# Optimization experiments

Hardware: AMD Instinct MI355X
Metric: run time of the kernel (lower is better)

## Reference

```python
import jax, jax.numpy as jnp
import numpy as np

HIGHEST = jax.lax.Precision.HIGHEST
KEY_CHUNK_SIZE = 4096 * 4  # hard-coded in the module's __call__
HEADS = 8
DIM_HEAD = 64


def _query_chunk_size(num_q: int) -> int:
    # replicates the module's static chunk-size selection
    if num_q % 64 == 0:
        return num_q // 64
    if num_q % 16 == 0:
        return num_q // 16
    if num_q % 4 == 0:
        return num_q // 4
    return num_q


def _me_attention(q, k, v, q_chunk: int, k_chunk: int):
    # q, k, v: (S, H, D) where H here is the flattened batch*heads axis
    S, H, D = q.shape
    num_kv = k.shape[0]
    k_chunk = min(k_chunk, num_kv)
    q = q / jnp.sqrt(jnp.asarray(D, q.dtype))
    kc = k.reshape(-1, k_chunk, H, D)          # (nk, kc, H, D)
    vc = v.reshape(-1, k_chunk, H, v.shape[-1])

    def per_qchunk(qch):  # qch: (qc, H, D)
        def summarize(args):
            kch, vch = args
            s = jnp.einsum('qhd,khd->qhk', qch, kch, precision=HIGHEST)
            m = jax.lax.stop_gradient(jnp.max(s, axis=-1, keepdims=True))
            e = jnp.exp(s - m)
            ev = jnp.einsum('khf,qhk->qhf', vch, e, precision=HIGHEST)
            return ev, e.sum(axis=-1), m[..., 0]
        evs, ews, ms = jax.lax.map(summarize, (kc, vc))  # stacked over key chunks
        gm = jnp.max(ms, axis=0)                # (qc, H) global running max
        sc = jnp.exp(ms - gm)                   # (nk, qc, H) rescale factors
        num = (evs * sc[..., None]).sum(axis=0)
        den = (ews * sc).sum(axis=0)
        return num / den[..., None]

    qs = q.reshape(-1, q_chunk, H, D)
    out = jax.lax.map(per_qchunk, qs)           # (nq, qc, H, F)
    return out.reshape(S, H, -1)


def _forward(hidden_states, w_q, w_k, w_v, w_out, b_out):
    B, S, Dm = hidden_states.shape
    H, dh = HEADS, DIM_HEAD
    q = hidden_states @ w_q
    k = hidden_states @ w_k
    v = hidden_states @ w_v

    def to_heads(t):  # (B,S,H*dh) -> (B*H, S, dh)
        return t.reshape(B, S, H, dh).transpose(0, 2, 1, 3).reshape(B * H, S, dh)

    qs, ks, vs = to_heads(q), to_heads(k), to_heads(v)
    # module transposes to (S, B*H, dh) before memory-efficient attention
    qcs = _query_chunk_size(S)
    attn = _me_attention(qs.transpose(1, 0, 2), ks.transpose(1, 0, 2),
                         vs.transpose(1, 0, 2), qcs, KEY_CHUNK_SIZE)
    attn = attn.transpose(1, 0, 2)  # (B*H, S, dh)
    attn = attn.reshape(B, H, S, dh).transpose(0, 2, 1, 3).reshape(B, S, H * dh)
    return attn @ w_out + b_out


def setup_inputs() -> dict:
    key = jax.random.key(0)
    ks = jax.random.split(key, 6)
    B, S, Dm = 2, 8192, 512
    inner = HEADS * DIM_HEAD  # 512
    return {
        'hidden_states': jax.random.normal(ks[0], (B, S, Dm), dtype=jnp.float32),
        'w_q': jax.random.normal(ks[1], (Dm, inner), dtype=jnp.float32) * 0.02,
        'w_k': jax.random.normal(ks[2], (Dm, inner), dtype=jnp.float32) * 0.02,
        'w_v': jax.random.normal(ks[3], (Dm, inner), dtype=jnp.float32) * 0.02,
        'w_out': jax.random.normal(ks[4], (inner, Dm), dtype=jnp.float32) * 0.02,
        'b_out': jnp.zeros((Dm,), dtype=jnp.float32),
    }


def reference(hidden_states, w_q, w_k, w_v, w_out, b_out):
    return _forward(hidden_states, w_q, w_k, w_v, w_out, b_out)
```

## Files before the change

### kernel.cpp

```cpp
#include <hip/hip_runtime.h>
#include <stdint.h>

typedef unsigned short u16;
typedef __attribute__((ext_vector_type(8))) short short8;
typedef __attribute__((ext_vector_type(4))) short short4v;
typedef __attribute__((ext_vector_type(4))) float f32x4;

#define MFMA16(a, b, c) __builtin_amdgcn_mfma_f32_16x16x16bf16_1k(a, b, c, 0, 0, 0)
#define MFMA32(a, b, c) __builtin_amdgcn_mfma_f32_16x16x32_bf16(a, b, c, 0, 0, 0)

#if __has_builtin(__builtin_amdgcn_exp2f)
#define EXP2F(x) __builtin_amdgcn_exp2f(x)
#else
#define EXP2F(x) exp2f(x)
#endif

#define ASYNC16(G, L)                                                            \
    __builtin_amdgcn_global_load_lds((const __attribute__((address_space(1))) void*)(const void*)(G), \
                                     (__attribute__((address_space(3))) void*)(void*)(L), 16, 0, 0)

__device__ __forceinline__ u16 f2bf(float f) {
    union { float f; uint32_t u; } c; c.f = f;
    uint32_t r = (c.u + 0x7fffu + ((c.u >> 16) & 1u)) >> 16;
    return (u16)r;
}

__global__ __launch_bounds__(256) void k_convert_x(const float* __restrict__ X, u16* __restrict__ Xb) {
    int idx = blockIdx.x * 256 + threadIdx.x;
    float4 v = ((const float4*)X)[idx];
    union { u16 s[4]; uint2 v; } u;
    u.s[0] = f2bf(v.x); u.s[1] = f2bf(v.y); u.s[2] = f2bf(v.z); u.s[3] = f2bf(v.w);
    ((uint2*)Xb)[idx] = u.v;
}

__global__ __launch_bounds__(256) void k_convert_w(const float* __restrict__ W0, const float* __restrict__ W1,
                                                   const float* __restrict__ W2, const float* __restrict__ W3,
                                                   u16* __restrict__ Wt) {
    __shared__ u16 T[64][72];
    const float* W = (blockIdx.z == 0) ? W0 : (blockIdx.z == 1) ? W1 : (blockIdx.z == 2) ? W2 : W3;
    int k0 = blockIdx.x * 64, n0 = blockIdx.y * 64;
    int t = threadIdx.x;
    for (int i = 0; i < 4; i++) {
        int id = t + i * 256;
        int row = id >> 4, c4 = (id & 15) * 4;
        float4 v = *(const float4*)(W + (size_t)(k0 + row) * 512 + n0 + c4);
        union { u16 s[4]; uint2 v; } u;
        u.s[0] = f2bf(v.x); u.s[1] = f2bf(v.y); u.s[2] = f2bf(v.z); u.s[3] = f2bf(v.w);
        *(uint2*)&T[row][c4] = u.v;
    }
    __syncthreads();
    u16* O = Wt + (size_t)blockIdx.z * 512 * 512;
    for (int i = 0; i < 2; i++) {
        int id = t + i * 256;
        int row = id >> 3, c8 = (id & 7) * 8;
        union { u16 s[8]; uint4 v; } tmp;
        for (int j = 0; j < 8; j++) tmp.s[j] = T[c8 + j][row];
        *(uint4*)(O + (size_t)(n0 + row) * 512 + k0 + c8) = tmp.v;
    }
}

__global__ __launch_bounds__(256) void k_gemm_qkv(const u16* __restrict__ X, const u16* __restrict__ Wt,
                                                  u16* __restrict__ Q, u16* __restrict__ K, u16* __restrict__ V) {
    __shared__ u16 As[128][40];
    __shared__ u16 Bs[128][40];
    const int t = threadIdx.x;
    const int wave = t >> 6, lane = t & 63, quad = lane >> 4, l16 = lane & 15;
    const int wm = (wave >> 1) * 64, wn = (wave & 1) * 64;
    const int m0 = blockIdx.x * 128, n0 = blockIdx.y * 128;
    const u16* Bt = Wt + (size_t)blockIdx.z * 262144;
    const f32x4 fz = {0.f, 0.f, 0.f, 0.f};
    f32x4 acc[4][4];
    for (int i = 0; i < 4; i++) for (int j = 0; j < 4; j++) acc[i][j] = fz;
    for (int k0 = 0; k0 < 512; k0 += 32) {
        __syncthreads();
        for (int i = 0; i < 2; i++) {
            int id = t + i * 256;
            int row = id >> 2, c8 = (id & 3) * 8;
            *(uint4*)&As[row][c8] = *(const uint4*)(X + (size_t)(m0 + row) * 512 + k0 + c8);
            *(uint4*)&Bs[row][c8] = *(const uint4*)(Bt + (size_t)(n0 + row) * 512 + k0 + c8);
        }
        __syncthreads();
        short8 af[4], bf[4];
        for (int mt = 0; mt < 4; mt++) af[mt] = *(const short8*)&As[wm + mt * 16 + l16][quad * 8];
        for (int nt = 0; nt < 4; nt++) bf[nt] = *(const short8*)&Bs[wn + nt * 16 + l16][quad * 8];
        for (int mt = 0; mt < 4; mt++)
            for (int nt = 0; nt < 4; nt++)
                acc[mt][nt] = MFMA32(af[mt], bf[nt], acc[mt][nt]);
    }
    const float scale = (blockIdx.z == 0) ? 0.18033688011112042f : 1.0f;
    u16* Out = (blockIdx.z == 0) ? Q : (blockIdx.z == 1) ? K : V;
    for (int mt = 0; mt < 4; mt++)
        for (int nt = 0; nt < 4; nt++)
            for (int r = 0; r < 4; r++) {
                int m = m0 + wm + mt * 16 + quad * 4 + r;
                int n = n0 + wn + nt * 16 + l16;
                int b = m >> 13, s = m & 8191, h = n >> 6, d = n & 63;
                Out[((size_t)((b * 8 + h) * 8192 + s)) * 64 + d] = f2bf(acc[mt][nt][r] * scale);
            }
}

__global__ __launch_bounds__(256) void k_transpose_v(const u16* __restrict__ V, u16* __restrict__ Vt) {
    __shared__ u16 T[64][72];
    int s0 = blockIdx.x * 64, bh = blockIdx.y;
    int t = threadIdx.x;
    for (int i = 0; i < 2; i++) {
        int id = t + i * 256, row = id >> 3, c8 = (id & 7) * 8;
        *(uint4*)&T[row][c8] = *(const uint4*)(V + ((size_t)bh * 8192 + s0 + row) * 64 + c8);
    }
    __syncthreads();
    for (int i = 0; i < 2; i++) {
        int id = t + i * 256, row = id >> 3, c8 = (id & 7) * 8;
        union { u16 s[8]; uint4 v; } tmp;
        for (int j = 0; j < 8; j++) tmp.s[j] = T[c8 + j][row];
        *(uint4*)(Vt + ((size_t)bh * 64 + row) * 8192 + s0 + c8) = tmp.v;
    }
}

__global__ __launch_bounds__(512, 4) void k_flash(const u16* __restrict__ Q, const u16* __restrict__ K,
                                                  const u16* __restrict__ Vt, u16* __restrict__ Attn) {
    __shared__ u16 KsAll[2][4096];
    __shared__ u16 VsAll[2][4096];
    const int t = threadIdx.x;
    const int wave = t >> 6, lane = t & 63, quad = lane >> 4, l16 = lane & 15;
    const int l7 = l16 & 7;
    const int qblk = blockIdx.x, bh = blockIdx.y;
    const int b = bh >> 3, h = bh & 7;
    const int q0g = qblk * 256;
    const int mq = wave * 32;
    const u16* Qb = Q + ((size_t)bh * 8192 + q0g) * 64;
    const u16* Kb = K + (size_t)bh * 8192 * 64;
    const u16* Vb = Vt + (size_t)bh * 64 * 8192;

    const int rA = ((l16 & 12) << 1) + (l16 & 3);

    const int r0 = t >> 3;
    const int x0K = ((t & 7) ^ ((r0 & 3) | ((r0 & 8) >> 1))) * 8;
    const int x0V = ((t & 7) ^ (r0 & 7)) * 8;
    const u16* gK0 = Kb + r0 * 64 + x0K;
    const u16* gV0 = Vb + (size_t)r0 * 8192 + x0V;
    u16* lK = &KsAll[0][0] + t * 8;
    u16* lV = &VsAll[0][0] + t * 8;

    auto prefetch = [&](int it, int buf) {
        ASYNC16(gK0 + it * 4096, lK + buf * 4096);
        ASYNC16(gV0 + it * 64,   lV + buf * 4096);
    };

    short8 qf[2][2];
    for (int mt = 0; mt < 2; mt++)
        for (int ks = 0; ks < 2; ks++)
            qf[mt][ks] = *(const short8*)(Qb + (size_t)(mq + mt * 16 + l16) * 64 + ks * 32 + quad * 8);

    const f32x4 fz = {0.f, 0.f, 0.f, 0.f};
    f32x4 o[2][4];
    float l_i[2] = {0.f, 0.f};
    for (int mt = 0; mt < 2; mt++) for (int nt = 0; nt < 4; nt++) o[mt][nt] = fz;

    prefetch(0, 0);

    auto body = [&](int it, int buf) {
        __syncthreads();
        if (it != 127) prefetch(it + 1, buf ^ 1);
        const u16* KsB = &KsAll[buf][0];
        const u16* VsB = &VsAll[buf][0];

        f32x4 scA[2][2], scB[2][2];
        for (int kg = 0; kg < 2; kg++) {
            const u16* KgA = KsB + kg * 2048 + rA * 64;
            const u16* KgB = KgA + 4 * 64;
            short8 a0 = *(const short8*)(KgA + ((0 * 4 + quad) ^ l7) * 8);
            short8 a1 = *(const short8*)(KgA + ((1 * 4 + quad) ^ l7) * 8);
            short8 b0 = *(const short8*)(KgB + ((0 * 4 + quad) ^ l7) * 8);
            short8 b1 = *(const short8*)(KgB + ((1 * 4 + quad) ^ l7) * 8);
            scA[0][kg] = MFMA32(a0, qf[0][0], fz);
            scA[1][kg] = MFMA32(a0, qf[1][0], fz);
            scB[0][kg] = MFMA32(b0, qf[0][0], fz);
            scB[1][kg] = MFMA32(b0, qf[1][0], fz);
            scA[0][kg] = MFMA32(a1, qf[0][1], scA[0][kg]);
            scA[1][kg] = MFMA32(a1, qf[1][1], scA[1][kg]);
            scB[0][kg] = MFMA32(b1, qf[0][1], scB[0][kg]);
            scB[1][kg] = MFMA32(b1, qf[1][1], scB[1][kg]);
        }

        short8 pf[2][2];
        for (int mt = 0; mt < 2; mt++)
            for (int kg = 0; kg < 2; kg++) {
                union { float f; uint32_t u; } eA0, eA1, eA2, eA3, eB0, eB1, eB2, eB3;
                eA0.f = EXP2F(scA[mt][kg][0]);
                eA1.f = EXP2F(scA[mt][kg][1]);
                eA2.f = EXP2F(scA[mt][kg][2]);
                eA3.f = EXP2F(scA[mt][kg][3]);
                eB0.f = EXP2F(scB[mt][kg][0]);
                eB1.f = EXP2F(scB[mt][kg][1]);
                eB2.f = EXP2F(scB[mt][kg][2]);
                eB3.f = EXP2F(scB[mt][kg][3]);
                l_i[mt] += ((eA0.f + eA1.f) + (eA2.f + eA3.f)) + ((eB0.f + eB1.f) + (eB2.f + eB3.f));
                union { uint32_t u[4]; short8 s; } pk;
                pk.u[0] = __builtin_amdgcn_perm(eA1.u, eA0.u, 0x07060302);
                pk.u[1] = __builtin_amdgcn_perm(eA3.u, eA2.u, 0x07060302);
                pk.u[2] = __builtin_amdgcn_perm(eB1.u, eB0.u, 0x07060302);
                pk.u[3] = __builtin_amdgcn_perm(eB3.u, eB2.u, 0x07060302);
                pf[mt][kg] = pk.s;
            }

        for (int kg = 0; kg < 2; kg++)
            for (int nt = 0; nt < 4; nt++) {
                short8 vf = *(const short8*)(VsB + nt * 1024 + l16 * 64 + (((kg * 4 + quad) ^ l7) * 8));
                o[0][nt] = MFMA32(pf[0][kg], vf, o[0][nt]);
                o[1][nt] = MFMA32(pf[1][kg], vf, o[1][nt]);
            }
    };

    for (int it2 = 0; it2 < 64; it2++) {
        body(2 * it2, 0);
        body(2 * it2 + 1, 1);
    }

    for (int mt = 0; mt < 2; mt++) {
        float l = l_i[mt];
        l += __shfl_xor(l, 16);
        l += __shfl_xor(l, 32);
        float inv = 1.0f / l;
        float invC[4];
        for (int r = 0; r < 4; r++) invC[r] = __shfl(inv, quad * 4 + r);
        for (int nt = 0; nt < 4; nt++)
            for (int r = 0; r < 4; r++) {
                int sg = q0g + mq + mt * 16 + quad * 4 + r;
                int n = h * 64 + nt * 16 + l16;
                Attn[((size_t)(b * 8192 + sg)) * 512 + n] = f2bf(o[mt][nt][r] * invC[r]);
            }
    }
}

__global__ __launch_bounds__(256) void k_gemm_out(const u16* __restrict__ A, const u16* __restrict__ Wot,
                                                  const float* __restrict__ bias, float* __restrict__ Out) {
    __shared__ u16 As[128][40];
    __shared__ u16 Bs[128][40];
    const int t = threadIdx.x;
    const int wave = t >> 6, lane = t & 63, quad = lane >> 4, l16 = lane & 15;
    const int wm = (wave >> 1) * 64, wn = (wave & 1) * 64;
    const int m0 = blockIdx.x * 128, n0 = blockIdx.y * 128;
    const f32x4 fz = {0.f, 0.f, 0.f, 0.f};
    f32x4 acc[4][4];
    for (int i = 0; i < 4; i++) for (int j = 0; j < 4; j++) acc[i][j] = fz;
    for (int k0 = 0; k0 < 512; k0 += 32) {
        __syncthreads();
        for (int i = 0; i < 2; i++) {
            int id = t + i * 256;
            int row = id >> 2, c8 = (id & 3) * 8;
            *(uint4*)&As[row][c8] = *(const uint4*)(A + (size_t)(m0 + row) * 512 + k0 + c8);
            *(uint4*)&Bs[row][c8] = *(const uint4*)(Wot + (size_t)(n0 + row) * 512 + k0 + c8);
        }
        __syncthreads();
        short8 af[4], bf[4];
        for (int mt = 0; mt < 4; mt++) af[mt] = *(const short8*)&As[wm + mt * 16 + l16][quad * 8];
        for (int nt = 0; nt < 4; nt++) bf[nt] = *(const short8*)&Bs[wn + nt * 16 + l16][quad * 8];
        for (int mt = 0; mt < 4; mt++)
            for (int nt = 0; nt < 4; nt++)
                acc[mt][nt] = MFMA32(af[mt], bf[nt], acc[mt][nt]);
    }
    float bv[4];
    for (int nt = 0; nt < 4; nt++) bv[nt] = bias[n0 + wn + nt * 16 + l16];
    for (int mt = 0; mt < 4; mt++)
        for (int nt = 0; nt < 4; nt++)
            for (int r = 0; r < 4; r++) {
                int m = m0 + wm + mt * 16 + quad * 4 + r;
                int n = n0 + wn + nt * 16 + l16;
                Out[(size_t)m * 512 + n] = acc[mt][nt][r] + bv[nt];
            }
}

extern "C" void kernel_launch(void* const* d_in, const int* in_sizes, int n_in,
                              void* d_out, int out_size, void* d_ws, size_t ws_size,
                              hipStream_t stream) {
    const float* X   = (const float*)d_in[0];
    const float* w_q = (const float*)d_in[1];
    const float* w_k = (const float*)d_in[2];
    const float* w_v = (const float*)d_in[3];
    const float* w_o = (const float*)d_in[4];
    const float* b_o = (const float*)d_in[5];
    float* Out = (float*)d_out;

    char* ws = (char*)d_ws;
    u16* Xb   = (u16*)(ws);
    u16* Wt   = (u16*)(ws + 16777216);
    u16* Qd   = (u16*)(ws + 18874368);
    u16* Kd   = (u16*)(ws + 35651584);
    u16* Vd   = (u16*)(ws + 52428800);
    u16* Vtd  = (u16*)(ws + 69206016);
    u16* Attn = Xb;

    hipLaunchKernelGGL(k_convert_x, dim3(8192), dim3(256), 0, stream, X, Xb);
    hipLaunchKernelGGL(k_convert_w, dim3(8, 8, 4), dim3(256), 0, stream, w_q, w_k, w_v, w_o, Wt);
    hipLaunchKernelGGL(k_gemm_qkv, dim3(128, 4, 3), dim3(256), 0, stream, Xb, Wt, Qd, Kd, Vd);
    hipLaunchKernelGGL(k_transpose_v, dim3(128, 16), dim3(256), 0, stream, Vd, Vtd);
    hipLaunchKernelGGL(k_flash, dim3(32, 16), dim3(512), 0, stream, Qd, Kd, Vtd, Attn);
    hipLaunchKernelGGL(k_gemm_out, dim3(128, 4), dim3(256), 0, stream, Attn, Wt + 3 * 262144, b_o, Out);
}
```

Measured before the change: 392.2 us.

## Process two key tiles per barrier and interleave QK, softmax, PV across them

The flash kernel's LDS staging grows from two to four buffers and loads two key/value tiles per prefetch, so there is one __syncthreads per pair of tiles instead of one per tile. Within each pair, the second tile's QK matmul is issued before the first tile's PV matmul, so exp2 work can overlap with MFMA. s_setprio is raised around the MFMA sections. LDS use per block doubles to 64KB, which may limit how many blocks fit per CU, and having two tiles live raises register pressure.

Result: slower. 1.036 ms (+164.1%).

```diff
diff --git a/kernel.cpp b/kernel.cpp
--- a/kernel.cpp
+++ b/kernel.cpp
@@ -6,7 +6,6 @@
 typedef __attribute__((ext_vector_type(4))) short short4v;
 typedef __attribute__((ext_vector_type(4))) float f32x4;
 
-#define MFMA16(a, b, c) __builtin_amdgcn_mfma_f32_16x16x16bf16_1k(a, b, c, 0, 0, 0)
 #define MFMA32(a, b, c) __builtin_amdgcn_mfma_f32_16x16x32_bf16(a, b, c, 0, 0, 0)
 
 #if __has_builtin(__builtin_amdgcn_exp2f)
@@ -118,8 +117,8 @@
 
 __global__ __launch_bounds__(512, 4) void k_flash(const u16* __restrict__ Q, const u16* __restrict__ K,
                                                   const u16* __restrict__ Vt, u16* __restrict__ Attn) {
-    __shared__ u16 KsAll[2][4096];
-    __shared__ u16 VsAll[2][4096];
+    __shared__ u16 KsAll[4][4096];
+    __shared__ u16 VsAll[4][4096];
     const int t = threadIdx.x;
     const int wave = t >> 6, lane = t & 63, quad = lane >> 4, l16 = lane & 15;
     const int l7 = l16 & 7;
@@ -141,9 +140,11 @@
     u16* lK = &KsAll[0][0] + t * 8;
     u16* lV = &VsAll[0][0] + t * 8;
 
-    auto prefetch = [&](int it, int buf) {
-        ASYNC16(gK0 + it * 4096, lK + buf * 4096);
-        ASYNC16(gV0 + it * 64,   lV + buf * 4096);
+    auto prefetch2 = [&](int it2, int pair) {
+        ASYNC16(gK0 + (2 * it2) * 4096,     lK + (pair * 2) * 4096);
+        ASYNC16(gK0 + (2 * it2 + 1) * 4096, lK + (pair * 2 + 1) * 4096);
+        ASYNC16(gV0 + (2 * it2) * 64,       lV + (pair * 2) * 4096);
+        ASYNC16(gV0 + (2 * it2 + 1) * 64,   lV + (pair * 2 + 1) * 4096);
     };
 
     short8 qf[2][2];
@@ -156,22 +157,16 @@
     float l_i[2] = {0.f, 0.f};
     for (int mt = 0; mt < 2; mt++) for (int nt = 0; nt < 4; nt++) o[mt][nt] = fz;
 
-    prefetch(0, 0);
-
-    auto body = [&](int it, int buf) {
-        __syncthreads();
-        if (it != 127) prefetch(it + 1, buf ^ 1);
-        const u16* KsB = &KsAll[buf][0];
-        const u16* VsB = &VsAll[buf][0];
-
-        f32x4 scA[2][2], scB[2][2];
+    auto qk_tile = [&](const u16* KsB, f32x4 (&scA)[2][2], f32x4 (&scB)[2][2]) {
+        __builtin_amdgcn_s_setprio(1);
+#pragma unroll
         for (int kg = 0; kg < 2; kg++) {
             const u16* KgA = KsB + kg * 2048 + rA * 64;
             const u16* KgB = KgA + 4 * 64;
-            short8 a0 = *(const short8*)(KgA + ((0 * 4 + quad) ^ l7) * 8);
-            short8 a1 = *(const short8*)(KgA + ((1 * 4 + quad) ^ l7) * 8);
-            short8 b0 = *(const short8*)(KgB + ((0 * 4 + quad) ^ l7) * 8);
-            short8 b1 = *(const short8*)(KgB + ((1 * 4 + quad) ^ l7) * 8);
+            short8 a0 = *(const short8*)(KgA + ((quad) ^ l7) * 8);
+            short8 a1 = *(const short8*)(KgA + ((4 + quad) ^ l7) * 8);
+            short8 b0 = *(const short8*)(KgB + ((quad) ^ l7) * 8);
+            short8 b1 = *(const short8*)(KgB + ((4 + quad) ^ l7) * 8);
             scA[0][kg] = MFMA32(a0, qf[0][0], fz);
             scA[1][kg] = MFMA32(a0, qf[1][0], fz);
             scB[0][kg] = MFMA32(b0, qf[0][0], fz);
@@ -181,9 +176,13 @@
             scB[0][kg] = MFMA32(b1, qf[0][1], scB[0][kg]);
             scB[1][kg] = MFMA32(b1, qf[1][1], scB[1][kg]);
         }
-
-        short8 pf[2][2];
+        __builtin_amdgcn_s_setprio(0);
+    };
+
+    auto sm_tile = [&](f32x4 (&scA)[2][2], f32x4 (&scB)[2][2], short8 (&pf)[2][2]) {
+#pragma unroll
         for (int mt = 0; mt < 2; mt++)
+#pragma unroll
             for (int kg = 0; kg < 2; kg++) {
                 union { float f; uint32_t u; } eA0, eA1, eA2, eA3, eB0, eB1, eB2, eB3;
                 eA0.f = EXP2F(scA[mt][kg][0]);
@@ -202,18 +201,40 @@
                 pk.u[3] = __builtin_amdgcn_perm(eB3.u, eB2.u, 0x07060302);
                 pf[mt][kg] = pk.s;
             }
-
+    };
+
+    auto pv_tile = [&](const u16* VsB, short8 (&pf)[2][2]) {
+        __builtin_amdgcn_s_setprio(1);
+#pragma unroll
         for (int kg = 0; kg < 2; kg++)
+#pragma unroll
             for (int nt = 0; nt < 4; nt++) {
                 short8 vf = *(const short8*)(VsB + nt * 1024 + l16 * 64 + (((kg * 4 + quad) ^ l7) * 8));
                 o[0][nt] = MFMA32(pf[0][kg], vf, o[0][nt]);
                 o[1][nt] = MFMA32(pf[1][kg], vf, o[1][nt]);
             }
+        __builtin_amdgcn_s_setprio(0);
     };
 
+    prefetch2(0, 0);
+
     for (int it2 = 0; it2 < 64; it2++) {
-        body(2 * it2, 0);
-        body(2 * it2 + 1, 1);
+        const int pair = it2 & 1;
+        __syncthreads();
+        if (it2 != 63) prefetch2(it2 + 1, pair ^ 1);
+        const u16* Ka = &KsAll[pair * 2][0];
+        const u16* Kc = &KsAll[pair * 2 + 1][0];
+        const u16* Va = &VsAll[pair * 2][0];
+        const u16* Vc = &VsAll[pair * 2 + 1][0];
+
+        f32x4 sA0[2][2], sB0[2][2], sA1[2][2], sB1[2][2];
+        short8 pf0[2][2], pf1[2][2];
+        qk_tile(Ka, sA0, sB0);
+        sm_tile(sA0, sB0, pf0);
+        qk_tile(Kc, sA1, sB1);
+        pv_tile(Va, pf0);
+        sm_tile(sA1, sB1, pf1);
+        pv_tile(Vc, pf1);
     }
 
     for (int mt = 0; mt < 2; mt++) {
```
